# Optimization experiments

Measured on AMD Instinct MI355X. Metric: run time of the kernel, lower is better.

Reference implementation:

```python
import jax, jax.numpy as jnp
import numpy as np

B, S, D = 2, 2048, 1024
H, KVH, HD = 16, 4, 64
ROPE_THETA = 10000.0


def rotate_half(x):
    h = x.shape[-1] // 2
    return jnp.concatenate([-x[..., h:], x[..., :h]], axis=-1)


def setup_inputs() -> dict:
    key = jax.random.key(0)
    k = jax.random.split(key, 6)
    x = jax.random.normal(k[0], (B, S, D), dtype=jnp.float32)
    # real RoPE tables: [S, HD//2]
    inv_freq = 1.0 / (ROPE_THETA ** (jnp.arange(0, HD, 2, dtype=jnp.float32) / HD))
    t = jnp.arange(S, dtype=jnp.float32)
    freqs = jnp.outer(t, inv_freq)  # [S, HD/2]
    cos = jnp.cos(freqs)
    sin = jnp.sin(freqs)
    # causal additive mask [1,1,S,S]
    neg = jnp.float32(-1e9)
    mask = jnp.where(jnp.tril(jnp.ones((S, S), dtype=bool)), 0.0, neg)[None, None]
    scale = 0.02
    wq = jax.random.normal(k[1], (D, H * HD), dtype=jnp.float32) * scale
    wk = jax.random.normal(k[2], (D, KVH * HD), dtype=jnp.float32) * scale
    wv = jax.random.normal(k[3], (D, KVH * HD), dtype=jnp.float32) * scale
    wo = jax.random.normal(k[4], (H * HD, D), dtype=jnp.float32) * scale
    return {"x": x, "cos": cos, "sin": sin, "mask": mask,
            "wq": wq, "wk": wk, "wv": wv, "wo": wo}


def reference(x, cos, sin, mask, wq, wk, wv, wo):
    b, s, d = x.shape
    hd = 2 * cos.shape[-1]
    h = wq.shape[1] // hd
    kvh = wk.shape[1] // hd
    n_rep = h // kvh

    q = (x @ wq).reshape(b, s, h, hd)
    k = (x @ wk).reshape(b, s, kvh, hd)
    v = (x @ wv).reshape(b, s, kvh, hd)

    # RoPE: cos/sin [S, hd/2] -> [1, s, 1, hd] via self-concat (rotate_half style)
    c = jnp.concatenate([cos[:s], cos[:s]], axis=-1)[None, :, None, :]
    sn = jnp.concatenate([sin[:s], sin[:s]], axis=-1)[None, :, None, :]
    q = q * c + rotate_half(q) * sn
    k = k * c + rotate_half(k) * sn

    new_k, new_v = k, v  # kv cache (pre-repeat)

    # GQA: repeat each kv head n_rep times contiguously (== expand+reshape)
    if n_rep > 1:
        k = jnp.repeat(k, n_rep, axis=2)
        v = jnp.repeat(v, n_rep, axis=2)

    scores = jnp.einsum('bqhd,bkhd->bhqk', q, k) / jnp.sqrt(jnp.float32(hd))
    scores = scores + mask
    attn = jax.nn.softmax(scores.astype(jnp.float32), axis=-1).astype(q.dtype)
    out = jnp.einsum('bhqk,bkhd->bqhd', attn, v).reshape(b, s, h * hd)
    out = out @ wo
    return (out, new_k, new_v)
```

## Files before the change

kernel.cpp:

```cpp
#include <hip/hip_runtime.h>
#include <hip/hip_bf16.h>

constexpr int B_ = 2, S_ = 2048, D_ = 1024, H_ = 16, KVH_ = 4, HD_ = 64;

typedef __attribute__((ext_vector_type(8))) short short8;
typedef __attribute__((ext_vector_type(4))) float f32x4;
typedef __attribute__((ext_vector_type(16))) float f32x16;

__device__ inline short f2b(float x) {
  unsigned u = __float_as_uint(x);
  return (short)((u + 0x7fffu + ((u >> 16) & 1u)) >> 16);
}
__device__ inline unsigned pkbf2(float lo, float hi) {
  __hip_bfloat162 h = __float22bfloat162_rn(float2{lo, hi});
  return *(unsigned*)&h;
}

__device__ inline void async16(void* lds, const void* g) {
  __builtin_amdgcn_global_load_lds(
      (const __attribute__((address_space(1))) unsigned int*)g,
      (__attribute__((address_space(3))) unsigned int*)lds, 16, 0, 0);
}

__global__ __launch_bounds__(256) void prep_kernel(
    const float* __restrict__ x, short* __restrict__ xb,
    const float* __restrict__ wq, const float* __restrict__ wk,
    const float* __restrict__ wv, const float* __restrict__ wo,
    short* __restrict__ wt, short* __restrict__ wot) {
  __shared__ short ts[64][66];
  const int tid = threadIdx.x;
  if (blockIdx.x < 4096) {
    const int idx = (blockIdx.x * 256 + tid) * 4;
    float4 v = *(const float4*)(x + idx);
    short4 o;
    o.x = f2b(v.x); o.y = f2b(v.y); o.z = f2b(v.z); o.w = f2b(v.w);
    *(short4*)(xb + idx) = o;
    return;
  }
  const int bid = blockIdx.x - 4096;
  const int z = bid >> 8, bi = (bid >> 4) & 15, bj = bid & 15;
  const float* W;
  short* dst;
  int N;
  if (z == 0)      { W = wq; dst = wt;                       N = 1024; }
  else if (z == 1) { W = wo; dst = wot;                      N = 1024; }
  else if (z == 2) { W = wk; dst = wt + (size_t)1024 * 1024; N = 256; }
  else             { W = wv; dst = wt + (size_t)1280 * 1024; N = 256; }
  if (bj * 64 >= N) return;
#pragma unroll
  for (int i = 0; i < 16; ++i) {
    int idx = tid + i * 256;
    int r = idx >> 6, c = idx & 63;
    ts[r][c] = f2b(W[(size_t)(bi * 64 + r) * N + bj * 64 + c]);
  }
  __syncthreads();
#pragma unroll
  for (int i = 0; i < 16; ++i) {
    int idx = tid + i * 256;
    int cc = idx >> 6, rr = idx & 63;
    dst[(size_t)(bj * 64 + cc) * 1024 + bi * 64 + rr] = ts[rr][cc];
  }
}

struct GemmLdsDb {
  short As[2][128][32];
  short Bs[2][128][32];
};

__device__ inline void gemm_core_db(GemmLdsDb& lds, const short* __restrict__ A,
                                    const short* __restrict__ Bt, int K,
                                    int row0, int col0, int tid,
                                    f32x4 (&acc)[4][4]) {
  const int w = tid >> 6, lane = tid & 63;
  const int grp = lane >> 4, li = lane & 15;
  const int wr = w & 1, wc = w >> 1;
  const int lr = lane >> 2, ls = (lane & 3) * 8;
#pragma unroll
  for (int mt = 0; mt < 4; ++mt)
#pragma unroll
    for (int nt = 0; nt < 4; ++nt) acc[mt][nt] = (f32x4){0.f, 0.f, 0.f, 0.f};

  auto issue = [&](int bi, int k0) {
#pragma unroll
    for (int i = 0; i < 2; ++i) {
      const int r = i * 64 + w * 16;
      async16(&lds.As[bi][r][0], A + (size_t)(row0 + r + lr) * K + k0 + ls);
      async16(&lds.Bs[bi][r][0], Bt + (size_t)(col0 + r + lr) * K + k0 + ls);
    }
  };

  issue(0, 0);
  const int nk = K >> 5;
  for (int kk = 0; kk < nk; ++kk) {
    const int cur = kk & 1;
    __syncthreads();
    if (kk + 1 < nk) issue(cur ^ 1, (kk + 1) << 5);

    short8 af[4], bf[4];
#pragma unroll
    for (int mt = 0; mt < 4; ++mt)
      af[mt] = *(const short8*)&lds.As[cur][wr * 64 + mt * 16 + li][grp * 8];
#pragma unroll
    for (int nt = 0; nt < 4; ++nt)
      bf[nt] = *(const short8*)&lds.Bs[cur][wc * 64 + nt * 16 + li][grp * 8];
#pragma unroll
    for (int mt = 0; mt < 4; ++mt)
#pragma unroll
      for (int nt = 0; nt < 4; ++nt)
        acc[mt][nt] = __builtin_amdgcn_mfma_f32_16x16x32_bf16(
            af[mt], bf[nt], acc[mt][nt], 0, 0, 0);
  }
}

#define QSCALE 0.1803368801111f

__global__ __launch_bounds__(256) void gemm_qkv(
    const short* __restrict__ A, const short* __restrict__ Bt,
    const float* __restrict__ cs, const float* __restrict__ sn,
    short* __restrict__ qb, float* __restrict__ koutp, short* __restrict__ kb,
    float* __restrict__ voutp, short* __restrict__ vbT) {
  __shared__ GemmLdsDb lds;
  const int tid = threadIdx.x;
  const int w = tid >> 6, lane = tid & 63;
  const int grp = lane >> 4, li = lane & 15;
  const int wr = w & 1, wc = w >> 1;
  const int row0 = blockIdx.y * 128, col0 = blockIdx.x * 128;
  f32x4 acc[4][4];
  gemm_core_db(lds, A, Bt, D_, row0, col0, tid, acc);

  if (col0 < 1024) {
#pragma unroll
    for (int mt = 0; mt < 4; ++mt)
#pragma unroll
      for (int r = 0; r < 4; ++r) {
        const int row = row0 + wr * 64 + mt * 16 + grp * 4 + r;
        const int spos = row & (S_ - 1);
#pragma unroll
        for (int nt = 0; nt < 2; ++nt) {
          const int col = col0 + wc * 64 + nt * 16 + li;
          const int d = col & 63;
          const float c = cs[spos * 32 + d];
          const float s = sn[spos * 32 + d];
          const float x0 = acc[mt][nt][r], x1 = acc[mt][nt + 2][r];
          qb[(size_t)row * 1024 + col] = f2b((x0 * c - x1 * s) * QSCALE);
          qb[(size_t)row * 1024 + col + 32] = f2b((x1 * c + x0 * s) * QSCALE);
        }
      }
  } else if (col0 < 1280) {
#pragma unroll
    for (int mt = 0; mt < 4; ++mt)
#pragma unroll
      for (int r = 0; r < 4; ++r) {
        const int row = row0 + wr * 64 + mt * 16 + grp * 4 + r;
        const int spos = row & (S_ - 1);
#pragma unroll
        for (int nt = 0; nt < 2; ++nt) {
          const int kcol = col0 + wc * 64 + nt * 16 + li - 1024;
          const int d = kcol & 63;
          const float c = cs[spos * 32 + d];
          const float s = sn[spos * 32 + d];
          const float x0 = acc[mt][nt][r], x1 = acc[mt][nt + 2][r];
          const float k0v = x0 * c - x1 * s;
          const float k1v = x1 * c + x0 * s;
          koutp[(size_t)row * 256 + kcol] = k0v;
          koutp[(size_t)row * 256 + kcol + 32] = k1v;
          kb[(size_t)row * 256 + kcol] = f2b(k0v);
          kb[(size_t)row * 256 + kcol + 32] = f2b(k1v);
        }
      }
  } else {
#pragma unroll
    for (int mt = 0; mt < 4; ++mt)
#pragma unroll
      for (int nt = 0; nt < 4; ++nt) {
        const int vcol = col0 + wc * 64 + nt * 16 + li - 1280;
        const int row_base = row0 + wr * 64 + mt * 16 + grp * 4;
        short4 pk;
        float vv[4];
#pragma unroll
        for (int r = 0; r < 4; ++r) vv[r] = acc[mt][nt][r];
        pk.x = f2b(vv[0]); pk.y = f2b(vv[1]);
        pk.z = f2b(vv[2]); pk.w = f2b(vv[3]);
#pragma unroll
        for (int r = 0; r < 4; ++r)
          voutp[(size_t)(row_base + r) * 256 + vcol] = vv[r];
        const int b = row_base >> 11, s0 = row_base & (S_ - 1);
        *(short4*)&vbT[((size_t)(b * 256 + vcol)) * S_ + s0] = pk;
      }
  }
}

struct KVT {
  short K[8][64][8];
  short V[8][64][8];
};

__global__ __launch_bounds__(256) void fattn_kernel(
    const short* __restrict__ qb, const short* __restrict__ kb,
    const short* __restrict__ vbT, short* __restrict__ o) {
  __shared__ KVT bufP[2][2];

  const int tid = threadIdx.x;
  const int w = tid >> 6, lane = tid & 63;
  const int n32 = lane & 31, kg = lane >> 5;
  const int st = w >> 1, par = w & 1;

  const int pr = blockIdx.x & 15;
  const int h = (blockIdx.x >> 4) & 15;
  const int b = blockIdx.x >> 8;
  const int kh = h >> 2;

  const short* kgp0 = kb + ((size_t)(b * S_) + lane) * 256 + kh * 64;
  const short* vgp0 = vbT + ((size_t)(b * 256 + kh * 64 + lane)) * S_;

  for (int pass = 0; pass < 2; ++pass) {
    const int qq = pass ? (31 - pr) : pr;
    const int nt = qq + 1, nph = (nt + 1) >> 1;
    const int qs0 = qq * 64 + st * 32;

    const short* qp =
        qb + (size_t)(b * S_ + qs0 + n32) * 1024 + h * 64 + kg * 8;
    short8 qa[4];
#pragma unroll
    for (int ks = 0; ks < 4; ++ks) qa[ks] = *(const short8*)(qp + ks * 16);

    f32x16 Oa0, Oa1;
#pragma unroll
    for (int i = 0; i < 16; ++i) { Oa0[i] = 0.f; Oa1[i] = 0.f; }
    float lreg = 0.f;

    auto issue = [&](int ph) {
      for (int tp = 0; tp < 2; ++tp) {
        const int t = 2 * ph + tp;
        if (t >= nt) break;
        KVT& d = bufP[ph & 1][tp];
        const short* kgp = kgp0 + (size_t)t * 16384;
        const short* vgp = vgp0 + t * 64;
        async16(&d.K[w][0][0], kgp + w * 8);
        async16(&d.K[w + 4][0][0], kgp + (w + 4) * 8);
        async16(&d.V[w][0][0], vgp + w * 8);
        async16(&d.V[w + 4][0][0], vgp + (w + 4) * 8);
      }
    };

    issue(0);
    for (int ph = 0; ph < nph; ++ph) {
      __syncthreads();
      if (ph + 1 < nph) issue(ph + 1);
      const int t = 2 * ph + par;
      if (t >= nt) continue;
      KVT& bf = bufP[ph & 1][par];
      const bool diag = (t == qq);

      unsigned pk[4][4];
#pragma unroll
      for (int s = 0; s < 2; ++s) {
        if (diag && st == 0 && s == 1) continue;
        f32x16 sv;
#pragma unroll
        for (int i = 0; i < 16; ++i) sv[i] = 0.f;
#pragma unroll
        for (int ks = 0; ks < 4; ++ks) {
          const short8 kf =
              *(const short8*)&bf.K[ks * 2 + kg][s * 32 + n32][0];
          sv = __builtin_amdgcn_mfma_f32_32x32x16_bf16(kf, qa[ks], sv, 0, 0, 0);
        }
        const bool dm = diag && (s == st);
        float p[16];
#pragma unroll
        for (int rr = 0; rr < 16; ++rr) {
          float e = exp2f(sv[rr]);
          if (dm) {
            const int key32 = (rr & 3) + 8 * (rr >> 2) + 4 * kg;
            if (key32 > n32) e = 0.f;
          }
          p[rr] = e;
          lreg += e;
        }
        pk[2 * s][0] = pkbf2(p[0], p[1]);
        pk[2 * s][1] = pkbf2(p[2], p[3]);
        pk[2 * s][2] = pkbf2(p[4], p[5]);
        pk[2 * s][3] = pkbf2(p[6], p[7]);
        pk[2 * s + 1][0] = pkbf2(p[8], p[9]);
        pk[2 * s + 1][1] = pkbf2(p[10], p[11]);
        pk[2 * s + 1][2] = pkbf2(p[12], p[13]);
        pk[2 * s + 1][3] = pkbf2(p[14], p[15]);
      }

      auto pv = [&](int kc) {
        const unsigned a0 = pk[kc][0], a1 = pk[kc][1];
        const unsigned b0 = pk[kc][2], b1 = pk[kc][3];
        const unsigned xa0 = (unsigned)__shfl_xor((int)a0, 32);
        const unsigned xa1 = (unsigned)__shfl_xor((int)a1, 32);
        const unsigned xb0 = (unsigned)__shfl_xor((int)b0, 32);
        const unsigned xb1 = (unsigned)__shfl_xor((int)b1, 32);
        union { unsigned u[4]; short8 s8; } f;
        f.u[0] = kg ? xb0 : a0;
        f.u[1] = kg ? xb1 : a1;
        f.u[2] = kg ? b0 : xa0;
        f.u[3] = kg ? b1 : xa1;
        const short8 v0 = *(const short8*)&bf.V[kc * 2 + kg][n32][0];
        const short8 v1 = *(const short8*)&bf.V[kc * 2 + kg][32 + n32][0];
        Oa0 = __builtin_amdgcn_mfma_f32_32x32x16_bf16(v0, f.s8, Oa0, 0, 0, 0);
        Oa1 = __builtin_amdgcn_mfma_f32_32x32x16_bf16(v1, f.s8, Oa1, 0, 0, 0);
      };
      if (diag && st == 0) {
        pv(0); pv(1);
      } else {
#pragma unroll
        for (int kc = 0; kc < 4; ++kc) pv(kc);
      }
    }

    lreg += __shfl_xor(lreg, 32);

    __syncthreads();
    float* scr = (float*)&bufP[0][0];
    float* lb = (float*)((char*)&bufP[0][0] + 16384);
    if (par == 1) {
#pragma unroll
      for (int rr = 0; rr < 16; ++rr) {
        const int d = (rr & 3) + 8 * (rr >> 2) + 4 * kg;
        scr[(st * 64 + d) * 32 + n32] = Oa0[rr];
        scr[(st * 64 + d + 32) * 32 + n32] = Oa1[rr];
      }
      if (kg == 0) lb[st * 32 + n32] = lreg;
    }
    __syncthreads();
    if (par == 0) {
      const float inv = 1.0f / (lreg + lb[st * 32 + n32]);
#pragma unroll
      for (int rr = 0; rr < 16; ++rr) {
        const int d = (rr & 3) + 8 * (rr >> 2) + 4 * kg;
        scr[(st * 64 + d) * 32 + n32] =
            (Oa0[rr] + scr[(st * 64 + d) * 32 + n32]) * inv;
        scr[(st * 64 + d + 32) * 32 + n32] =
            (Oa1[rr] + scr[(st * 64 + d + 32) * 32 + n32]) * inv;
      }
    }
    __syncthreads();
    {
      const int ql = tid >> 2, dseg = (tid & 3) * 16;
      const size_t gb = (size_t)(b * S_ + qq * 64 + ql) * 1024 + h * 64 + dseg;
      short8 t0, t1;
#pragma unroll
      for (int k2 = 0; k2 < 8; ++k2) {
        t0[k2] = f2b(scr[((ql >> 5) * 64 + dseg + k2) * 32 + (ql & 31)]);
        t1[k2] = f2b(scr[((ql >> 5) * 64 + dseg + 8 + k2) * 32 + (ql & 31)]);
      }
      *(short8*)(o + gb) = t0;
      *(short8*)(o + gb + 8) = t1;
    }
    __syncthreads();
  }
}

__global__ __launch_bounds__(256) void gemm_bt_f32(
    const short* __restrict__ A, const short* __restrict__ Bt,
    float* __restrict__ C, int N, int K) {
  __shared__ GemmLdsDb lds;
  const int tid = threadIdx.x;
  const int w = tid >> 6, lane = tid & 63;
  const int grp = lane >> 4, li = lane & 15;
  const int wr = w & 1, wc = w >> 1;
  const int row0 = blockIdx.y * 128, col0 = blockIdx.x * 128;
  f32x4 acc[4][4];
  gemm_core_db(lds, A, Bt, K, row0, col0, tid, acc);
#pragma unroll
  for (int mt = 0; mt < 4; ++mt)
#pragma unroll
    for (int nt = 0; nt < 4; ++nt)
#pragma unroll
      for (int r = 0; r < 4; ++r)
        C[(size_t)(row0 + wr * 64 + mt * 16 + grp * 4 + r) * N + col0 +
          wc * 64 + nt * 16 + li] = acc[mt][nt][r];
}

extern "C" void kernel_launch(void* const* d_in, const int* in_sizes, int n_in,
                              void* d_out, int out_size, void* d_ws,
                              size_t ws_size, hipStream_t stream) {
  const float* x  = (const float*)d_in[0];
  const float* cs = (const float*)d_in[1];
  const float* sn = (const float*)d_in[2];
  const float* wq = (const float*)d_in[4];
  const float* wk = (const float*)d_in[5];
  const float* wv = (const float*)d_in[6];
  const float* wo = (const float*)d_in[7];

  float* outp  = (float*)d_out;
  float* koutp = outp + (size_t)B_ * S_ * H_ * HD_;
  float* voutp = koutp + (size_t)B_ * S_ * KVH_ * HD_;

  char* p = (char*)d_ws;
  short* xb   = (short*)p; p += (size_t)B_ * S_ * D_ * 2;
  short* qb   = (short*)p; p += (size_t)B_ * S_ * H_ * HD_ * 2;
  short* kb   = (short*)p; p += (size_t)B_ * S_ * KVH_ * HD_ * 2;
  short* vbT  = (short*)p; p += (size_t)B_ * S_ * KVH_ * HD_ * 2;
  short* abuf = (short*)p; p += (size_t)B_ * S_ * H_ * HD_ * 2;
  short* wt   = (short*)p; p += (size_t)1536 * D_ * 2;
  short* wot  = (short*)p; p += (size_t)D_ * H_ * HD_ * 2;

  const int M = B_ * S_;

  prep_kernel<<<4096 + 1024, 256, 0, stream>>>(x, xb, wq, wk, wv, wo, wt,
                                               wot);

  gemm_qkv<<<dim3(1536 / 128, M / 128), 256, 0, stream>>>(
      xb, wt, cs, sn, qb, koutp, kb, voutp, vbT);

  fattn_kernel<<<B_ * H_ * 16, 256, 0, stream>>>(qb, kb, vbT, abuf);

  gemm_bt_f32<<<dim3(1024 / 128, M / 128), 256, 0, stream>>>(abuf, wot, outp,
                                                             1024, 1024);
}
```

Measured before the change: 192.0 us.

## Restructure flash attention into small per-32-query blocks reading K/V from global

The attention kernel moves from 256-thread blocks that handle paired 64-row query tiles (for causal balance) with double-buffered async LDS staging of K/V to 128-thread blocks, each handling one 32-query tile. K and V fragments are loaded directly from global memory (L2/cache) instead of through LDS, and blocks are ordered longest-first. The half-wave exchange now uses permlane32_swap in place of shuffles, exp2 and reciprocal use the raw hardware builtins, and the LDS scratch is padded to 33 columns. Launching more, smaller blocks without barriers is meant to raise occupancy and remove the sync overhead, at the cost of losing LDS reuse of K/V across waves and relying on the cache.

```diff
diff --git a/kernel.cpp b/kernel.cpp
--- a/kernel.cpp
+++ b/kernel.cpp
@@ -190,168 +190,136 @@
   }
 }
 
-struct KVT {
-  short K[8][64][8];
-  short V[8][64][8];
-};
-
-__global__ __launch_bounds__(256) void fattn_kernel(
+__global__ __launch_bounds__(128) void fattn_kernel(
     const short* __restrict__ qb, const short* __restrict__ kb,
     const short* __restrict__ vbT, short* __restrict__ o) {
-  __shared__ KVT bufP[2][2];
+  __shared__ float scr[64 * 33 + 32];
 
   const int tid = threadIdx.x;
-  const int w = tid >> 6, lane = tid & 63;
+  const int par = tid >> 6, lane = tid & 63;
   const int n32 = lane & 31, kg = lane >> 5;
-  const int st = w >> 1, par = w & 1;
-
-  const int pr = blockIdx.x & 15;
-  const int h = (blockIdx.x >> 4) & 15;
-  const int b = blockIdx.x >> 8;
-  const int kh = h >> 2;
-
-  const short* kgp0 = kb + ((size_t)(b * S_) + lane) * 256 + kh * 64;
-  const short* vgp0 = vbT + ((size_t)(b * 256 + kh * 64 + lane)) * S_;
-
-  for (int pass = 0; pass < 2; ++pass) {
-    const int qq = pass ? (31 - pr) : pr;
-    const int nt = qq + 1, nph = (nt + 1) >> 1;
-    const int qs0 = qq * 64 + st * 32;
-
-    const short* qp =
-        qb + (size_t)(b * S_ + qs0 + n32) * 1024 + h * 64 + kg * 8;
-    short8 qa[4];
-#pragma unroll
-    for (int ks = 0; ks < 4; ++ks) qa[ks] = *(const short8*)(qp + ks * 16);
-
-    f32x16 Oa0, Oa1;
-#pragma unroll
-    for (int i = 0; i < 16; ++i) { Oa0[i] = 0.f; Oa1[i] = 0.f; }
-    float lreg = 0.f;
-
-    auto issue = [&](int ph) {
-      for (int tp = 0; tp < 2; ++tp) {
-        const int t = 2 * ph + tp;
-        if (t >= nt) break;
-        KVT& d = bufP[ph & 1][tp];
-        const short* kgp = kgp0 + (size_t)t * 16384;
-        const short* vgp = vgp0 + t * 64;
-        async16(&d.K[w][0][0], kgp + w * 8);
-        async16(&d.K[w + 4][0][0], kgp + (w + 4) * 8);
-        async16(&d.V[w][0][0], vgp + w * 8);
-        async16(&d.V[w + 4][0][0], vgp + (w + 4) * 8);
+
+  const int qt = 63 - (blockIdx.x >> 5);
+  const int bh = blockIdx.x & 31;
+  const int b = bh >> 4, h = bh & 15, kh = h >> 2;
+  const int qq = qt >> 1, st = qt & 1;
+  const int nt = qq + 1;
+
+  const short* qp =
+      qb + ((size_t)(b * S_ + qt * 32 + n32)) * 1024 + h * 64 + kg * 8;
+  short8 qa[4];
+#pragma unroll
+  for (int ks = 0; ks < 4; ++ks) qa[ks] = *(const short8*)(qp + ks * 16);
+
+  const short* kl = kb + ((size_t)(b * S_) + n32) * 256 + kh * 64 + kg * 8;
+  const short* vl0 = vbT + ((size_t)(b * 256 + kh * 64 + n32)) * S_ + kg * 8;
+  const short* vl1 = vl0 + (size_t)32 * S_;
+
+  f32x16 zero16;
+#pragma unroll
+  for (int i = 0; i < 16; ++i) zero16[i] = 0.f;
+  f32x16 Oa0 = zero16, Oa1 = zero16;
+  float lreg = 0.f;
+
+  for (int t = par; t < nt; t += 2) {
+    const bool diag = (t == qq);
+    const short* kt = kl + (size_t)t * (64 * 256);
+    const short* vt0 = vl0 + t * 64;
+    const short* vt1 = vl1 + t * 64;
+    unsigned pk[4][4];
+
+#pragma unroll
+    for (int s = 0; s < 2; ++s) {
+      if (s == 1 && diag && st == 0) continue;
+      const short* krow = kt + s * (32 * 256);
+      const short8 kf0 = *(const short8*)(krow);
+      const short8 kf1 = *(const short8*)(krow + 16);
+      const short8 kf2 = *(const short8*)(krow + 32);
+      const short8 kf3 = *(const short8*)(krow + 48);
+      f32x16 sv =
+          __builtin_amdgcn_mfma_f32_32x32x16_bf16(kf0, qa[0], zero16, 0, 0, 0);
+      sv = __builtin_amdgcn_mfma_f32_32x32x16_bf16(kf1, qa[1], sv, 0, 0, 0);
+      sv = __builtin_amdgcn_mfma_f32_32x32x16_bf16(kf2, qa[2], sv, 0, 0, 0);
+      sv = __builtin_amdgcn_mfma_f32_32x32x16_bf16(kf3, qa[3], sv, 0, 0, 0);
+
+      const bool dm = diag && (s == st);
+      float e[16];
+#pragma unroll
+      for (int rr = 0; rr < 16; ++rr) {
+        float v = __builtin_amdgcn_exp2f(sv[rr]);
+        if (dm) {
+          const int key32 = (rr & 3) + 8 * (rr >> 2) + 4 * kg;
+          if (key32 > n32) v = 0.f;
+        }
+        e[rr] = v;
       }
+      pk[2 * s][0] = pkbf2(e[0], e[1]);
+      pk[2 * s][1] = pkbf2(e[2], e[3]);
+      pk[2 * s][2] = pkbf2(e[4], e[5]);
+      pk[2 * s][3] = pkbf2(e[6], e[7]);
+      pk[2 * s + 1][0] = pkbf2(e[8], e[9]);
+      pk[2 * s + 1][1] = pkbf2(e[10], e[11]);
+      pk[2 * s + 1][2] = pkbf2(e[12], e[13]);
+      pk[2 * s + 1][3] = pkbf2(e[14], e[15]);
+      lreg += (((e[0] + e[1]) + (e[2] + e[3])) +
+               ((e[4] + e[5]) + (e[6] + e[7]))) +
+              (((e[8] + e[9]) + (e[10] + e[11])) +
+               ((e[12] + e[13]) + (e[14] + e[15])));
+    }
+
+    auto pv = [&](int kc) {
+      auto r02 = __builtin_amdgcn_permlane32_swap(pk[kc][0], pk[kc][2],
+                                                  false, false);
+      auto r13 = __builtin_amdgcn_permlane32_swap(pk[kc][1], pk[kc][3],
+                                                  false, false);
+      union { unsigned u[4]; short8 s8; } f;
+      f.u[0] = r02[0]; f.u[1] = r13[0]; f.u[2] = r02[1]; f.u[3] = r13[1];
+      const short8 v0 = *(const short8*)(vt0 + kc * 16);
+      const short8 v1 = *(const short8*)(vt1 + kc * 16);
+      Oa0 = __builtin_amdgcn_mfma_f32_32x32x16_bf16(v0, f.s8, Oa0, 0, 0, 0);
+      Oa1 = __builtin_amdgcn_mfma_f32_32x32x16_bf16(v1, f.s8, Oa1, 0, 0, 0);
     };
-
-    issue(0);
-    for (int ph = 0; ph < nph; ++ph) {
-      __syncthreads();
-      if (ph + 1 < nph) issue(ph + 1);
-      const int t = 2 * ph + par;
-      if (t >= nt) continue;
-      KVT& bf = bufP[ph & 1][par];
-      const bool diag = (t == qq);
-
-      unsigned pk[4][4];
-#pragma unroll
-      for (int s = 0; s < 2; ++s) {
-        if (diag && st == 0 && s == 1) continue;
-        f32x16 sv;
-#pragma unroll
-        for (int i = 0; i < 16; ++i) sv[i] = 0.f;
-#pragma unroll
-        for (int ks = 0; ks < 4; ++ks) {
-          const short8 kf =
-              *(const short8*)&bf.K[ks * 2 + kg][s * 32 + n32][0];
-          sv = __builtin_amdgcn_mfma_f32_32x32x16_bf16(kf, qa[ks], sv, 0, 0, 0);
-        }
-        const bool dm = diag && (s == st);
-        float p[16];
-#pragma unroll
-        for (int rr = 0; rr < 16; ++rr) {
-          float e = exp2f(sv[rr]);
-          if (dm) {
-            const int key32 = (rr & 3) + 8 * (rr >> 2) + 4 * kg;
-            if (key32 > n32) e = 0.f;
-          }
-          p[rr] = e;
-          lreg += e;
-        }
-        pk[2 * s][0] = pkbf2(p[0], p[1]);
-        pk[2 * s][1] = pkbf2(p[2], p[3]);
-        pk[2 * s][2] = pkbf2(p[4], p[5]);
-        pk[2 * s][3] = pkbf2(p[6], p[7]);
-        pk[2 * s + 1][0] = pkbf2(p[8], p[9]);
-        pk[2 * s + 1][1] = pkbf2(p[10], p[11]);
-        pk[2 * s + 1][2] = pkbf2(p[12], p[13]);
-        pk[2 * s + 1][3] = pkbf2(p[14], p[15]);
-      }
-
-      auto pv = [&](int kc) {
-        const unsigned a0 = pk[kc][0], a1 = pk[kc][1];
-        const unsigned b0 = pk[kc][2], b1 = pk[kc][3];
-        const unsigned xa0 = (unsigned)__shfl_xor((int)a0, 32);
-        const unsigned xa1 = (unsigned)__shfl_xor((int)a1, 32);
-        const unsigned xb0 = (unsigned)__shfl_xor((int)b0, 32);
-        const unsigned xb1 = (unsigned)__shfl_xor((int)b1, 32);
-        union { unsigned u[4]; short8 s8; } f;
-        f.u[0] = kg ? xb0 : a0;
-        f.u[1] = kg ? xb1 : a1;
-        f.u[2] = kg ? b0 : xa0;
-        f.u[3] = kg ? b1 : xa1;
-        const short8 v0 = *(const short8*)&bf.V[kc * 2 + kg][n32][0];
-        const short8 v1 = *(const short8*)&bf.V[kc * 2 + kg][32 + n32][0];
-        Oa0 = __builtin_amdgcn_mfma_f32_32x32x16_bf16(v0, f.s8, Oa0, 0, 0, 0);
-        Oa1 = __builtin_amdgcn_mfma_f32_32x32x16_bf16(v1, f.s8, Oa1, 0, 0, 0);
-      };
-      if (diag && st == 0) {
-        pv(0); pv(1);
-      } else {
-#pragma unroll
-        for (int kc = 0; kc < 4; ++kc) pv(kc);
-      }
-    }
-
-    lreg += __shfl_xor(lreg, 32);
-
-    __syncthreads();
-    float* scr = (float*)&bufP[0][0];
-    float* lb = (float*)((char*)&bufP[0][0] + 16384);
-    if (par == 1) {
-#pragma unroll
-      for (int rr = 0; rr < 16; ++rr) {
-        const int d = (rr & 3) + 8 * (rr >> 2) + 4 * kg;
-        scr[(st * 64 + d) * 32 + n32] = Oa0[rr];
-        scr[(st * 64 + d + 32) * 32 + n32] = Oa1[rr];
-      }
-      if (kg == 0) lb[st * 32 + n32] = lreg;
-    }
-    __syncthreads();
-    if (par == 0) {
-      const float inv = 1.0f / (lreg + lb[st * 32 + n32]);
-#pragma unroll
-      for (int rr = 0; rr < 16; ++rr) {
-        const int d = (rr & 3) + 8 * (rr >> 2) + 4 * kg;
-        scr[(st * 64 + d) * 32 + n32] =
-            (Oa0[rr] + scr[(st * 64 + d) * 32 + n32]) * inv;
-        scr[(st * 64 + d + 32) * 32 + n32] =
-            (Oa1[rr] + scr[(st * 64 + d + 32) * 32 + n32]) * inv;
-      }
-    }
-    __syncthreads();
-    {
-      const int ql = tid >> 2, dseg = (tid & 3) * 16;
-      const size_t gb = (size_t)(b * S_ + qq * 64 + ql) * 1024 + h * 64 + dseg;
-      short8 t0, t1;
-#pragma unroll
-      for (int k2 = 0; k2 < 8; ++k2) {
-        t0[k2] = f2b(scr[((ql >> 5) * 64 + dseg + k2) * 32 + (ql & 31)]);
-        t1[k2] = f2b(scr[((ql >> 5) * 64 + dseg + 8 + k2) * 32 + (ql & 31)]);
-      }
-      *(short8*)(o + gb) = t0;
-      *(short8*)(o + gb + 8) = t1;
-    }
-    __syncthreads();
+    if (diag && st == 0) {
+      pv(0); pv(1);
+    } else {
+      pv(0); pv(1); pv(2); pv(3);
+    }
+  }
+
+  lreg += __shfl_xor(lreg, 32);
+
+  float* lb = scr + 64 * 33;
+  if (par == 1) {
+#pragma unroll
+    for (int rr = 0; rr < 16; ++rr) {
+      const int d0 = (rr & 3) + 8 * (rr >> 2) + 4 * kg;
+      scr[d0 * 33 + n32] = Oa0[rr];
+      scr[(d0 + 32) * 33 + n32] = Oa1[rr];
+    }
+    if (kg == 0) lb[n32] = lreg;
+  }
+  __syncthreads();
+  if (par == 0) {
+    const float inv = __builtin_amdgcn_rcpf(lreg + lb[n32]);
+#pragma unroll
+    for (int rr = 0; rr < 16; ++rr) {
+      const int d0 = (rr & 3) + 8 * (rr >> 2) + 4 * kg;
+      scr[d0 * 33 + n32] = (Oa0[rr] + scr[d0 * 33 + n32]) * inv;
+      scr[(d0 + 32) * 33 + n32] = (Oa1[rr] + scr[(d0 + 32) * 33 + n32]) * inv;
+    }
+  }
+  __syncthreads();
+  {
+    const int q = tid >> 2, seg = (tid & 3) * 16;
+    const size_t gb = ((size_t)(b * S_ + qt * 32 + q)) * 1024 + h * 64 + seg;
+    short8 t0, t1;
+#pragma unroll
+    for (int k2 = 0; k2 < 8; ++k2) {
+      t0[k2] = f2b(scr[(seg + k2) * 33 + q]);
+      t1[k2] = f2b(scr[(seg + 8 + k2) * 33 + q]);
+    }
+    *(short8*)(o + gb) = t0;
+    *(short8*)(o + gb + 8) = t1;
   }
 }
 
@@ -408,7 +376,7 @@
   gemm_qkv<<<dim3(1536 / 128, M / 128), 256, 0, stream>>>(
       xb, wt, cs, sn, qb, koutp, kb, voutp, vbT);
 
-  fattn_kernel<<<B_ * H_ * 16, 256, 0, stream>>>(qb, kb, vbT, abuf);
+  fattn_kernel<<<64 * 32, 128, 0, stream>>>(qb, kb, vbT, abuf);
 
   gemm_bt_f32<<<dim3(1024 / 128, M / 128), 256, 0, stream>>>(abuf, wot, outp,
                                                              1024, 1024);
```

New measurement: 206.3 us. 1.07x slower.
